# Kernel optimization log

Hardware: AMD Instinct MI355X
Metric: run time of the kernel (lower is better)

Reference implementation:

```python
import jax, jax.numpy as jnp
import numpy as np

CV_CHAN = 49  # displacement channels; radius = (CV_CHAN - 1) // 2 = 24


def conv1x1(x, W, b):
    # x: [B,C,H,Wd], W: [O,C], b: [O] -> [B,O,H,Wd]
    return jnp.einsum('oc,bchw->bohw', W, x) + b[None, :, None, None]


def corr_volume(f1, f2, radius, eps):
    """Shift-and-dot correlation along width. f1,f2: [B,C,H,W] -> [B,2r+1,H,W].
    Channel k corresponds to displacement d = k - radius; out-of-range positions are 0
    (handled by zero-padding, matching the torch zero-filled shifted tensors)."""
    f1n = f1 / (jnp.linalg.norm(f1, axis=1, keepdims=True) + eps)
    f2n = f2 / (jnp.linalg.norm(f2, axis=1, keepdims=True) + eps)
    Wd = f1.shape[3]
    pad = jnp.pad(f2n, ((0, 0), (0, 0), (0, 0), (radius, radius)))
    # shifted_k[x] = f2n[x - d] = pad[x + 2*radius - k]
    slices = [
        jnp.sum(f1n * jax.lax.dynamic_slice_in_dim(pad, 2 * radius - k, Wd, axis=3), axis=1)
        for k in range(2 * radius + 1)
    ]
    return jnp.stack(slices, axis=1)


def setup_inputs() -> dict:
    key = jax.random.key(0)
    ks = jax.random.split(key, 10)
    B, C, H, W = 4, 128, 128, 256
    F = 128  # fmap channels
    G = 96   # geo encoder output channels
    s = 0.05
    return {
        'feat_l1': jax.random.normal(ks[0], (B, C, H, W), jnp.float32),
        'feat_r1': jax.random.normal(ks[1], (B, C, H, W), jnp.float32),
        'cv0': jax.random.normal(ks[2], (B, CV_CHAN, H, W), jnp.float32),
        'cv1': jax.random.normal(ks[3], (B, CV_CHAN, H, W), jnp.float32),
        'cv2': jax.random.normal(ks[4], (B, CV_CHAN, H, W), jnp.float32),
        'W_f1': jax.random.normal(ks[5], (F, C), jnp.float32) * s,
        'b_f1': jnp.zeros((F,), jnp.float32),
        'W_f2': jax.random.normal(ks[6], (F, C), jnp.float32) * s,
        'b_f2': jnp.zeros((F,), jnp.float32),
        'W_geo': jax.random.normal(ks[7], (G, CV_CHAN), jnp.float32) * s,
        'b_geo': jnp.zeros((G,), jnp.float32),
        'W_sel': jax.random.normal(ks[8], (3, 3 * G), jnp.float32) * s,
        'b_sel': jnp.zeros((3,), jnp.float32),
    }


def reference(feat_l1, feat_r1, cv0, cv1, cv2,
              W_f1, b_f1, W_f2, b_f2, W_geo, b_geo, W_sel, b_sel):
    # init feature maps (init_fmap1 / init_fmap2 as 1x1 convs)
    fmap1 = conv1x1(feat_l1, W_f1, b_f1)
    fmap2 = conv1x1(feat_r1, W_f2, b_f2)
    radius = (CV_CHAN - 1) // 2
    init_corr = corr_volume(fmap1, fmap2, radius, 1e-8)  # [B, CV_CHAN, H, W]

    # geo_volume2 (1x1 conv CV_CHAN -> 96) applied to each geometric volume
    g0 = conv1x1(cv0, W_geo, b_geo)
    g1 = conv1x1(cv1, W_geo, b_geo)
    g2 = conv1x1(cv2, W_geo, b_geo)
    combined_g = jnp.concatenate([g0, g1, g2], axis=1)  # [B, 288, H, W]

    logits = conv1x1(combined_g, W_sel, b_sel)           # [B, 3, H, W]
    w = jax.nn.softmax(logits, axis=1)

    weighted = (w[:, 0:1] * cv0[:, :CV_CHAN]
                + w[:, 1:2] * cv1[:, :CV_CHAN]
                + w[:, 2:3] * cv2[:, :CV_CHAN])
    final = init_corr + weighted
    return (final, init_corr, w)
```

## Files before the change

kernel.cpp:

```cpp
#include <hip/hip_runtime.h>

#define HW 32768
#define WIDTH 256

typedef float f32x4 __attribute__((ext_vector_type(4)));
typedef short s16x8 __attribute__((ext_vector_type(8)));

__device__ __forceinline__ unsigned short f2bf(float f){
    unsigned int u = __float_as_uint(f);
    u += 0x7FFFu + ((u >> 16) & 1u);
    return (unsigned short)(u >> 16);
}
__device__ __forceinline__ unsigned int pk2(float a, float b){
    return (unsigned int)f2bf(a) | ((unsigned int)f2bf(b) << 16);
}

__global__ __launch_bounds__(256, 2) void k_fmap(
    const float* __restrict__ fl, const float* __restrict__ fr,
    const float* __restrict__ W1, const float* __restrict__ W2,
    const float* __restrict__ b1, const float* __restrict__ b2,
    unsigned short* __restrict__ f1N, unsigned short* __restrict__ f2N)
{
    const int z = blockIdx.z;
    const float* feat = z ? fr : fl;
    const float* Wm   = z ? W2 : W1;
    const float* bias = z ? b2 : b1;
    unsigned short* out = z ? f2N : f1N;

    const int b    = blockIdx.y;
    const int pxb  = blockIdx.x * 256;
    const int tid  = threadIdx.x;
    const int wv   = tid >> 6;
    const int lane = tid & 63;
    const int quad = lane >> 4;
    const int l15  = lane & 15;

    f32x4 acc[8][4];
    #pragma unroll
    for (int m = 0; m < 8; ++m)
        #pragma unroll
        for (int nt = 0; nt < 4; ++nt)
            acc[m][nt] = (f32x4){0.f,0.f,0.f,0.f};

    const float* featB = feat + (size_t)b * 128 * HW + pxb;

    #pragma unroll
    for (int kk = 0; kk < 4; ++kk){
        const int kc0 = kk * 32;

        s16x8 af[8];
        #pragma unroll
        for (int m = 0; m < 8; ++m){
            const float* wp = Wm + (m * 16 + l15) * 128 + kc0 + quad * 8;
            f32x4 w0 = *(const f32x4*)wp;
            f32x4 w1 = *(const f32x4*)(wp + 4);
            union { unsigned int u[4]; s16x8 v; } r;
            r.u[0] = pk2(w0[0], w0[1]); r.u[1] = pk2(w0[2], w0[3]);
            r.u[2] = pk2(w1[0], w1[1]); r.u[3] = pk2(w1[2], w1[3]);
            af[m] = r.v;
        }

        #pragma unroll
        for (int nt = 0; nt < 4; ++nt){
            const int px = wv * 64 + nt * 16 + l15;
            const float* bp = featB + (size_t)(kc0 + quad * 8) * HW + px;
            float x[8];
            #pragma unroll
            for (int j = 0; j < 8; ++j)
                x[j] = bp[(size_t)j * HW];
            union { unsigned int u[4]; s16x8 v; } r;
            r.u[0] = pk2(x[0], x[1]); r.u[1] = pk2(x[2], x[3]);
            r.u[2] = pk2(x[4], x[5]); r.u[3] = pk2(x[6], x[7]);
            const s16x8 bf = r.v;
            #pragma unroll
            for (int m = 0; m < 8; ++m)
                acc[m][nt] = __builtin_amdgcn_mfma_f32_16x16x32_bf16(af[m], bf, acc[m][nt], 0, 0, 0);
        }
    }

    __shared__ unsigned short Ts[64][132];

    for (int nt = 0; nt < 4; ++nt){
        __syncthreads();
        #pragma unroll
        for (int m = 0; m < 8; ++m){
            f32x4 bv = *(const f32x4*)(bias + m * 16 + quad * 4);
            acc[m][nt] += bv;
        }
        float n2 = 0.f;
        #pragma unroll
        for (int m = 0; m < 8; ++m)
            #pragma unroll
            for (int r = 0; r < 4; ++r)
                n2 += acc[m][nt][r] * acc[m][nt][r];
        n2 += __shfl_xor(n2, 16, 64);
        n2 += __shfl_xor(n2, 32, 64);
        const float scale = 1.f / (sqrtf(n2) + 1e-8f);

        unsigned short* trow = &Ts[wv * 16 + l15][0];
        #pragma unroll
        for (int m = 0; m < 8; ++m){
            uint2 pk;
            pk.x = pk2(acc[m][nt][0] * scale, acc[m][nt][1] * scale);
            pk.y = pk2(acc[m][nt][2] * scale, acc[m][nt][3] * scale);
            *(uint2*)(trow + m * 16 + quad * 4) = pk;
        }
        __syncthreads();

        const int s  = tid >> 2;
        const int ch = tid & 3;
        const int wvs = s >> 4, ls = s & 15;
        const int gpx = pxb + wvs * 64 + nt * 16 + ls;
        const unsigned short* src = &Ts[s][ch * 32];
        unsigned short* dst = out + ((size_t)b * HW + gpx) * 128 + ch * 32;
        #pragma unroll
        for (int i = 0; i < 4; ++i){
            union { struct { uint2 a, c; } p; s16x8 v; } m;
            m.p.a = *(const uint2*)(src + i * 8);
            m.p.c = *(const uint2*)(src + i * 8 + 4);
            *(s16x8*)(dst + i * 8) = m.v;
        }
    }
}

__global__ __launch_bounds__(256, 4) void k_corr(
    const unsigned short* __restrict__ f1N,
    const unsigned short* __restrict__ f2N,
    float* __restrict__ ic)
{
    const int tid  = threadIdx.x;
    const int wv   = tid >> 6;
    const int lane = tid & 63;
    const int quad = lane >> 4;
    const int l15  = lane & 15;

    const int strip = blockIdx.x * 4 + wv;
    const int b   = strip >> 11;
    const int rem = strip & 2047;
    const int h   = rem >> 4;
    const int x0  = (rem & 15) << 4;

    const size_t rowbase = (size_t)b * HW + (size_t)h * WIDTH;

    const unsigned short* arow = f1N + (rowbase + x0 + l15) * 128;
    s16x8 af[4];
    #pragma unroll
    for (int kk = 0; kk < 4; ++kk)
        af[kk] = *(const s16x8*)(arow + kk * 32 + quad * 8);

    f32x4 acc[4];
    #pragma unroll
    for (int nt = 0; nt < 4; ++nt) acc[nt] = (f32x4){0.f,0.f,0.f,0.f};

    #pragma unroll
    for (int nt = 0; nt < 4; ++nt){
        const int s = x0 + nt * 16 + l15 - 24;
        const bool valid = (s >= 0) && (s < WIDTH);
        const unsigned short* brow = f2N + (rowbase + s) * 128;
        #pragma unroll
        for (int kk = 0; kk < 4; ++kk){
            s16x8 bf = (s16x8){0,0,0,0,0,0,0,0};
            if (valid) bf = *(const s16x8*)(brow + kk * 32 + quad * 8);
            acc[nt] = __builtin_amdgcn_mfma_f32_16x16x32_bf16(af[kk], bf, acc[nt], 0, 0, 0);
        }
    }

    __shared__ float G[4][16][68];
    #pragma unroll
    for (int nt = 0; nt < 4; ++nt)
        #pragma unroll
        for (int r = 0; r < 4; ++r)
            G[wv][quad * 4 + r][nt * 16 + l15] = acc[nt][r];
    __syncthreads();

    float* obase = ic + (size_t)b * 49 * HW + (size_t)h * WIDTH + x0;
    #pragma unroll
    for (int i = 0; i < 13; ++i){
        int dd = quad + i * 4;
        if (dd < 49){
            float v = G[wv][l15][l15 + 48 - dd];
            obase[(size_t)dd * HW + l15] = v;
        }
    }
}

__global__ void k_prep(const float* __restrict__ Wsel, const float* __restrict__ bsel,
                       const float* __restrict__ Wgeo, const float* __restrict__ bgeo,
                       float* __restrict__ M, float* __restrict__ c0)
{
    int u = threadIdx.x;
    if (u < 441){
        int s = u / 147; int r = u % 147; int i = r / 49; int k = r % 49;
        float acc = 0.f;
        for (int o = 0; o < 96; ++o)
            acc += Wsel[s * 288 + i * 96 + o] * Wgeo[o * 49 + k];
        M[u] = acc;
    } else if (u < 444){
        int s = u - 441;
        float acc = bsel[s];
        for (int i = 0; i < 3; ++i)
            for (int o = 0; o < 96; ++o)
                acc += Wsel[s * 288 + i * 96 + o] * bgeo[o];
        c0[s] = acc;
    }
}

__global__ __launch_bounds__(256, 2) void k_sel(
    const float* __restrict__ cv0, const float* __restrict__ cv1, const float* __restrict__ cv2,
    const float* __restrict__ M, const float* __restrict__ c0,
    const float* __restrict__ ic,
    float* __restrict__ finalO, float* __restrict__ wO)
{
    __shared__ float Ms[441];
    __shared__ float c0s[3];
    const int tid = threadIdx.x;
    for (int i = tid; i < 441; i += 256) Ms[i] = M[i];
    if (tid < 3) c0s[tid] = c0[tid];
    __syncthreads();

    const int gid = blockIdx.x * 256 + tid;
    const int b = gid >> 15;
    const int p = gid & 32767;
    const size_t base = (size_t)b * 49 * HW + p;

    float a0[49], a1[49], a2[49];
    #pragma unroll
    for (int k = 0; k < 49; ++k){
        size_t o = base + (size_t)k * HW;
        a0[k] = cv0[o]; a1[k] = cv1[o]; a2[k] = cv2[o];
    }

    float lg0 = c0s[0], lg1 = c0s[1], lg2 = c0s[2];
    #pragma unroll
    for (int k = 0; k < 49; ++k){
        lg0 += Ms[k]       * a0[k] + Ms[49  + k] * a1[k] + Ms[98  + k] * a2[k];
        lg1 += Ms[147 + k] * a0[k] + Ms[196 + k] * a1[k] + Ms[245 + k] * a2[k];
        lg2 += Ms[294 + k] * a0[k] + Ms[343 + k] * a1[k] + Ms[392 + k] * a2[k];
    }
    float mx = fmaxf(lg0, fmaxf(lg1, lg2));
    float e0 = expf(lg0 - mx), e1 = expf(lg1 - mx), e2 = expf(lg2 - mx);
    float inv = 1.f / (e0 + e1 + e2);
    float w0 = e0 * inv, w1 = e1 * inv, w2 = e2 * inv;

    const size_t wbase = (size_t)b * 3 * HW + p;
    wO[wbase]          = w0;
    wO[wbase + HW]     = w1;
    wO[wbase + 2 * HW] = w2;

    #pragma unroll
    for (int k = 0; k < 49; ++k){
        size_t o = base + (size_t)k * HW;
        finalO[o] = ic[o] + w0 * a0[k] + w1 * a1[k] + w2 * a2[k];
    }
}

extern "C" void kernel_launch(void* const* d_in, const int* in_sizes, int n_in,
                              void* d_out, int out_size, void* d_ws, size_t ws_size,
                              hipStream_t stream)
{
    const float* feat_l1 = (const float*)d_in[0];
    const float* feat_r1 = (const float*)d_in[1];
    const float* cv0     = (const float*)d_in[2];
    const float* cv1     = (const float*)d_in[3];
    const float* cv2     = (const float*)d_in[4];
    const float* W_f1    = (const float*)d_in[5];
    const float* b_f1    = (const float*)d_in[6];
    const float* W_f2    = (const float*)d_in[7];
    const float* b_f2    = (const float*)d_in[8];
    const float* W_geo   = (const float*)d_in[9];
    const float* b_geo   = (const float*)d_in[10];
    const float* W_sel   = (const float*)d_in[11];
    const float* b_sel   = (const float*)d_in[12];

    float* finalO = (float*)d_out;
    float* icO    = (float*)d_out + 6422528;
    float* wO     = (float*)d_out + 12845056;

    unsigned short* f1N = (unsigned short*)d_ws;
    unsigned short* f2N = (unsigned short*)((char*)d_ws + 33554432);
    float* Mbuf  = (float*)((char*)d_ws + 67108864);
    float* c0buf = Mbuf + 441;

    k_prep<<<1, 512, 0, stream>>>(W_sel, b_sel, W_geo, b_geo, Mbuf, c0buf);
    k_fmap<<<dim3(128, 4, 2), 256, 0, stream>>>(feat_l1, feat_r1, W_f1, W_f2, b_f1, b_f2, f1N, f2N);
    k_corr<<<2048, 256, 0, stream>>>(f1N, f2N, icO);
    k_sel<<<512, 256, 0, stream>>>(cv0, cv1, cv2, Mbuf, c0buf, icO, finalO, wO);
}
```

Before: 301.7 us.

## Fuse fmap projection and correlation into one per-row kernel via LDS

Merges the 1x1 feature projection and the correlation kernels into a single kernel where each block handles one image row. fmap1 stays in registers and is redistributed with shuffles, while fmap2 is staged in LDS. Normalization is applied as per-pixel scale factors on the correlation output, so the bf16 intermediate tensors no longer make a global-memory round trip. Weights are staged in LDS and the next feature loads are software-prefetched. The cost is a grid of only 512 blocks, heavy LDS use (about 66KB per block), and more register pressure, which may lower occupancy.

```diff
diff --git a/kernel.cpp b/kernel.cpp
--- a/kernel.cpp
+++ b/kernel.cpp
@@ -15,171 +15,213 @@
     return (unsigned int)f2bf(a) | ((unsigned int)f2bf(b) << 16);
 }
 
-__global__ __launch_bounds__(256, 2) void k_fmap(
+__global__ __launch_bounds__(256, 2) void k_fused(
     const float* __restrict__ fl, const float* __restrict__ fr,
     const float* __restrict__ W1, const float* __restrict__ W2,
     const float* __restrict__ b1, const float* __restrict__ b2,
-    unsigned short* __restrict__ f1N, unsigned short* __restrict__ f2N)
+    float* __restrict__ ic)
 {
-    const int z = blockIdx.z;
-    const float* feat = z ? fr : fl;
-    const float* Wm   = z ? W2 : W1;
-    const float* bias = z ? b2 : b1;
-    unsigned short* out = z ? f2N : f1N;
-
-    const int b    = blockIdx.y;
-    const int pxb  = blockIdx.x * 256;
+    __shared__ char pool[67584];
+    __shared__ float s1[256], s2[256];
+    unsigned short* Wlds = (unsigned short*)pool;
+    unsigned short* f2s  = (unsigned short*)pool;
+    float* G             = (float*)pool;
+
+    const int blk  = blockIdx.x;
+    const int b    = blk >> 7;
+    const int h    = blk & 127;
     const int tid  = threadIdx.x;
     const int wv   = tid >> 6;
     const int lane = tid & 63;
     const int quad = lane >> 4;
     const int l15  = lane & 15;
 
-    f32x4 acc[8][4];
-    #pragma unroll
-    for (int m = 0; m < 8; ++m)
-        #pragma unroll
-        for (int nt = 0; nt < 4; ++nt)
-            acc[m][nt] = (f32x4){0.f,0.f,0.f,0.f};
-
-    const float* featB = feat + (size_t)b * 128 * HW + pxb;
-
-    #pragma unroll
-    for (int kk = 0; kk < 4; ++kk){
-        const int kc0 = kk * 32;
-
-        s16x8 af[8];
-        #pragma unroll
-        for (int m = 0; m < 8; ++m){
-            const float* wp = Wm + (m * 16 + l15) * 128 + kc0 + quad * 8;
-            f32x4 w0 = *(const f32x4*)wp;
-            f32x4 w1 = *(const f32x4*)(wp + 4);
+    const float* feats[2] = { fl + (size_t)b * 128 * HW + h * WIDTH,
+                              fr + (size_t)b * 128 * HW + h * WIDTH };
+    const float* Wms[2]   = { W1, W2 };
+    const float* bss[2]   = { b1, b2 };
+
+    unsigned int f1p[64];
+
+    #pragma unroll 1
+    for (int F = 0; F < 2; ++F){
+        const float* featB = feats[F];
+        const float* Wm    = Wms[F];
+        const float* bias  = bss[F];
+
+        __syncthreads();
+        {
+            const int r = tid >> 1, c0 = (tid & 1) * 64;
+            #pragma unroll
+            for (int i = 0; i < 16; ++i){
+                f32x4 v = *(const f32x4*)(Wm + r * 128 + c0 + i * 4);
+                uint2 p; p.x = pk2(v[0], v[1]); p.y = pk2(v[2], v[3]);
+                *(uint2*)&Wlds[r * 132 + c0 + i * 4] = p;
+            }
+        }
+        __syncthreads();
+
+        f32x4 acc[8][4];
+        #pragma unroll
+        for (int m = 0; m < 8; ++m)
+            #pragma unroll
+            for (int nt = 0; nt < 4; ++nt)
+                acc[m][nt] = (f32x4){0.f, 0.f, 0.f, 0.f};
+
+        float cur[8], nxt[8];
+        {
+            const float* bp = featB + (size_t)(quad * 8) * HW + wv * 64 + l15;
+            #pragma unroll
+            for (int j = 0; j < 8; ++j) cur[j] = bp[(size_t)j * HW];
+        }
+
+        #pragma unroll
+        for (int kk = 0; kk < 4; ++kk){
+            s16x8 af[8];
+            #pragma unroll
+            for (int m = 0; m < 8; ++m){
+                const int base = (m * 16 + l15) * 132 + kk * 32 + quad * 8;
+                union { uint2 q2[2]; s16x8 v; } r;
+                r.q2[0] = *(const uint2*)&Wlds[base];
+                r.q2[1] = *(const uint2*)&Wlds[base + 4];
+                af[m] = r.v;
+            }
+            #pragma unroll
+            for (int nt = 0; nt < 4; ++nt){
+                const int kn  = kk + ((nt + 1) >> 2);
+                const int ntn = (nt + 1) & 3;
+                if (kn < 4){
+                    const float* bp = featB + (size_t)(kn * 32 + quad * 8) * HW
+                                      + wv * 64 + ntn * 16 + l15;
+                    #pragma unroll
+                    for (int j = 0; j < 8; ++j) nxt[j] = bp[(size_t)j * HW];
+                }
+                union { unsigned int u[4]; s16x8 v; } rb;
+                rb.u[0] = pk2(cur[0], cur[1]); rb.u[1] = pk2(cur[2], cur[3]);
+                rb.u[2] = pk2(cur[4], cur[5]); rb.u[3] = pk2(cur[6], cur[7]);
+                #pragma unroll
+                for (int m = 0; m < 8; ++m)
+                    acc[m][nt] = __builtin_amdgcn_mfma_f32_16x16x32_bf16(af[m], rb.v, acc[m][nt], 0, 0, 0);
+                #pragma unroll
+                for (int j = 0; j < 8; ++j) cur[j] = nxt[j];
+            }
+        }
+
+        float inv[4];
+        #pragma unroll
+        for (int nt = 0; nt < 4; ++nt){
+            #pragma unroll
+            for (int m = 0; m < 8; ++m)
+                acc[m][nt] += *(const f32x4*)(bias + m * 16 + quad * 4);
+            float n2 = 0.f;
+            #pragma unroll
+            for (int m = 0; m < 8; ++m)
+                #pragma unroll
+                for (int r = 0; r < 4; ++r)
+                    n2 += acc[m][nt][r] * acc[m][nt][r];
+            n2 += __shfl_xor(n2, 16, 64);
+            n2 += __shfl_xor(n2, 32, 64);
+            inv[nt] = 1.f / (sqrtf(n2) + 1e-8f);
+        }
+
+        if (F == 0){
+            #pragma unroll
+            for (int m = 0; m < 8; ++m)
+                #pragma unroll
+                for (int nt = 0; nt < 4; ++nt){
+                    f1p[m * 8 + nt * 2 + 0] = pk2(acc[m][nt][0], acc[m][nt][1]);
+                    f1p[m * 8 + nt * 2 + 1] = pk2(acc[m][nt][2], acc[m][nt][3]);
+                }
+            if (quad == 0){
+                #pragma unroll
+                for (int nt = 0; nt < 4; ++nt) s1[wv * 64 + nt * 16 + l15] = inv[nt];
+            }
+        } else {
+            if (quad == 0){
+                #pragma unroll
+                for (int nt = 0; nt < 4; ++nt) s2[wv * 64 + nt * 16 + l15] = inv[nt];
+            }
+            __syncthreads();
+            #pragma unroll
+            for (int nt = 0; nt < 4; ++nt){
+                const int px = wv * 64 + nt * 16 + l15;
+                #pragma unroll
+                for (int m = 0; m < 8; ++m){
+                    uint2 p;
+                    p.x = pk2(acc[m][nt][0], acc[m][nt][1]);
+                    p.y = pk2(acc[m][nt][2], acc[m][nt][3]);
+                    *(uint2*)&f2s[px * 132 + m * 16 + quad * 4] = p;
+                }
+            }
+        }
+    }
+    __syncthreads();
+
+    f32x4 acc_c[4][4];
+    #pragma unroll
+    for (int st = 0; st < 4; ++st)
+        #pragma unroll
+        for (int ct = 0; ct < 4; ++ct)
+            acc_c[st][ct] = (f32x4){0.f, 0.f, 0.f, 0.f};
+
+    #pragma unroll
+    for (int st = 0; st < 4; ++st){
+        s16x8 afc[4];
+        #pragma unroll
+        for (int kk = 0; kk < 4; ++kk){
             union { unsigned int u[4]; s16x8 v; } r;
-            r.u[0] = pk2(w0[0], w0[1]); r.u[1] = pk2(w0[2], w0[3]);
-            r.u[2] = pk2(w1[0], w1[1]); r.u[3] = pk2(w1[2], w1[3]);
-            af[m] = r.v;
-        }
-
-        #pragma unroll
-        for (int nt = 0; nt < 4; ++nt){
-            const int px = wv * 64 + nt * 16 + l15;
-            const float* bp = featB + (size_t)(kc0 + quad * 8) * HW + px;
-            float x[8];
-            #pragma unroll
-            for (int j = 0; j < 8; ++j)
-                x[j] = bp[(size_t)j * HW];
-            union { unsigned int u[4]; s16x8 v; } r;
-            r.u[0] = pk2(x[0], x[1]); r.u[1] = pk2(x[2], x[3]);
-            r.u[2] = pk2(x[4], x[5]); r.u[3] = pk2(x[6], x[7]);
-            const s16x8 bf = r.v;
-            #pragma unroll
-            for (int m = 0; m < 8; ++m)
-                acc[m][nt] = __builtin_amdgcn_mfma_f32_16x16x32_bf16(af[m], bf, acc[m][nt], 0, 0, 0);
-        }
-    }
-
-    __shared__ unsigned short Ts[64][132];
-
-    for (int nt = 0; nt < 4; ++nt){
-        __syncthreads();
-        #pragma unroll
-        for (int m = 0; m < 8; ++m){
-            f32x4 bv = *(const f32x4*)(bias + m * 16 + quad * 4);
-            acc[m][nt] += bv;
-        }
-        float n2 = 0.f;
-        #pragma unroll
-        for (int m = 0; m < 8; ++m)
+            #pragma unroll
+            for (int j2 = 0; j2 < 4; ++j2){
+                const int rp  = j2 & 1;
+                const int qs  = (quad & 1) * 2 + (j2 >> 1);
+                const int src = qs * 16 + l15;
+                unsigned int a0 = (unsigned int)__shfl((int)f1p[(kk * 2 + 0) * 8 + st * 2 + rp], src, 64);
+                unsigned int a1 = (unsigned int)__shfl((int)f1p[(kk * 2 + 1) * 8 + st * 2 + rp], src, 64);
+                r.u[j2] = (quad >> 1) ? a1 : a0;
+            }
+            afc[kk] = r.v;
+        }
+        #pragma unroll
+        for (int ct = 0; ct < 4; ++ct){
+            const int s = wv * 64 + st * 16 + ct * 16 + l15 - 24;
+            const bool valid = (s >= 0) && (s < WIDTH);
+            const int sc = valid ? s : 0;
+            #pragma unroll
+            for (int kk = 0; kk < 4; ++kk){
+                union { uint2 q2[2]; s16x8 v; } rb;
+                rb.q2[0] = *(const uint2*)&f2s[sc * 132 + kk * 32 + quad * 8];
+                rb.q2[1] = *(const uint2*)&f2s[sc * 132 + kk * 32 + quad * 8 + 4];
+                s16x8 bf = rb.v;
+                if (!valid) bf = (s16x8){0,0,0,0,0,0,0,0};
+                acc_c[st][ct] = __builtin_amdgcn_mfma_f32_16x16x32_bf16(afc[kk], bf, acc_c[st][ct], 0, 0, 0);
+            }
+        }
+    }
+    __syncthreads();
+    #pragma unroll
+    for (int st = 0; st < 4; ++st)
+        #pragma unroll
+        for (int ct = 0; ct < 4; ++ct)
             #pragma unroll
             for (int r = 0; r < 4; ++r)
-                n2 += acc[m][nt][r] * acc[m][nt][r];
-        n2 += __shfl_xor(n2, 16, 64);
-        n2 += __shfl_xor(n2, 32, 64);
-        const float scale = 1.f / (sqrtf(n2) + 1e-8f);
-
-        unsigned short* trow = &Ts[wv * 16 + l15][0];
-        #pragma unroll
-        for (int m = 0; m < 8; ++m){
-            uint2 pk;
-            pk.x = pk2(acc[m][nt][0] * scale, acc[m][nt][1] * scale);
-            pk.y = pk2(acc[m][nt][2] * scale, acc[m][nt][3] * scale);
-            *(uint2*)(trow + m * 16 + quad * 4) = pk;
-        }
-        __syncthreads();
-
-        const int s  = tid >> 2;
-        const int ch = tid & 3;
-        const int wvs = s >> 4, ls = s & 15;
-        const int gpx = pxb + wvs * 64 + nt * 16 + ls;
-        const unsigned short* src = &Ts[s][ch * 32];
-        unsigned short* dst = out + ((size_t)b * HW + gpx) * 128 + ch * 32;
-        #pragma unroll
-        for (int i = 0; i < 4; ++i){
-            union { struct { uint2 a, c; } p; s16x8 v; } m;
-            m.p.a = *(const uint2*)(src + i * 8);
-            m.p.c = *(const uint2*)(src + i * 8 + 4);
-            *(s16x8*)(dst + i * 8) = m.v;
-        }
-    }
-}
-
-__global__ __launch_bounds__(256, 4) void k_corr(
-    const unsigned short* __restrict__ f1N,
-    const unsigned short* __restrict__ f2N,
-    float* __restrict__ ic)
-{
-    const int tid  = threadIdx.x;
-    const int wv   = tid >> 6;
-    const int lane = tid & 63;
-    const int quad = lane >> 4;
-    const int l15  = lane & 15;
-
-    const int strip = blockIdx.x * 4 + wv;
-    const int b   = strip >> 11;
-    const int rem = strip & 2047;
-    const int h   = rem >> 4;
-    const int x0  = (rem & 15) << 4;
-
-    const size_t rowbase = (size_t)b * HW + (size_t)h * WIDTH;
-
-    const unsigned short* arow = f1N + (rowbase + x0 + l15) * 128;
-    s16x8 af[4];
-    #pragma unroll
-    for (int kk = 0; kk < 4; ++kk)
-        af[kk] = *(const s16x8*)(arow + kk * 32 + quad * 8);
-
-    f32x4 acc[4];
-    #pragma unroll
-    for (int nt = 0; nt < 4; ++nt) acc[nt] = (f32x4){0.f,0.f,0.f,0.f};
-
-    #pragma unroll
-    for (int nt = 0; nt < 4; ++nt){
-        const int s = x0 + nt * 16 + l15 - 24;
-        const bool valid = (s >= 0) && (s < WIDTH);
-        const unsigned short* brow = f2N + (rowbase + s) * 128;
-        #pragma unroll
-        for (int kk = 0; kk < 4; ++kk){
-            s16x8 bf = (s16x8){0,0,0,0,0,0,0,0};
-            if (valid) bf = *(const s16x8*)(brow + kk * 32 + quad * 8);
-            acc[nt] = __builtin_amdgcn_mfma_f32_16x16x32_bf16(af[kk], bf, acc[nt], 0, 0, 0);
-        }
-    }
-
-    __shared__ float G[4][16][68];
-    #pragma unroll
-    for (int nt = 0; nt < 4; ++nt)
-        #pragma unroll
-        for (int r = 0; r < 4; ++r)
-            G[wv][quad * 4 + r][nt * 16 + l15] = acc[nt][r];
+                G[((wv * 4 + st) * 16 + quad * 4 + r) * 66 + ct * 16 + l15] = acc_c[st][ct][r];
     __syncthreads();
 
-    float* obase = ic + (size_t)b * 49 * HW + (size_t)h * WIDTH + x0;
-    #pragma unroll
-    for (int i = 0; i < 13; ++i){
-        int dd = quad + i * 4;
-        if (dd < 49){
-            float v = G[wv][l15][l15 + 48 - dd];
-            obase[(size_t)dd * HW + l15] = v;
+    float* obase = ic + (size_t)b * 49 * HW + (size_t)h * WIDTH;
+    #pragma unroll
+    for (int st = 0; st < 4; ++st){
+        const int gx = wv * 64 + st * 16;
+        const float sc1 = s1[gx + l15];
+        const float* Grow = &G[((wv * 4 + st) * 16 + l15) * 66];
+        #pragma unroll
+        for (int i = 0; i < 13; ++i){
+            const int dd = quad + i * 4;
+            if (dd < 49){
+                int s2i = gx + l15 + 24 - dd;
+                s2i = s2i < 0 ? 0 : (s2i > 255 ? 255 : s2i);
+                const float v = Grow[l15 + 48 - dd] * sc1 * s2[s2i];
+                obase[(size_t)dd * HW + gx + l15] = v;
+            }
         }
     }
 }
@@ -276,13 +318,10 @@
     float* icO    = (float*)d_out + 6422528;
     float* wO     = (float*)d_out + 12845056;
 
-    unsigned short* f1N = (unsigned short*)d_ws;
-    unsigned short* f2N = (unsigned short*)((char*)d_ws + 33554432);
-    float* Mbuf  = (float*)((char*)d_ws + 67108864);
+    float* Mbuf  = (float*)d_ws;
     float* c0buf = Mbuf + 441;
 
     k_prep<<<1, 512, 0, stream>>>(W_sel, b_sel, W_geo, b_geo, Mbuf, c0buf);
-    k_fmap<<<dim3(128, 4, 2), 256, 0, stream>>>(feat_l1, feat_r1, W_f1, W_f2, b_f1, b_f2, f1N, f2N);
-    k_corr<<<2048, 256, 0, stream>>>(f1N, f2N, icO);
+    k_fused<<<512, 256, 0, stream>>>(feat_l1, feat_r1, W_f1, W_f2, b_f1, b_f2, icO);
     k_sel<<<512, 256, 0, stream>>>(cv0, cv1, cv2, Mbuf, c0buf, icO, finalO, wO);
 }
```

After: 281.0 us. 1.07x faster.
